# Performance work log

Measured on AMD Instinct MI355X. Metric: run time of the kernel, lower is better.

## Reference

```python
import jax, jax.numpy as jnp
import numpy as np

B, T, C = 256, 512, 128


def setup_inputs() -> dict:
    key = jax.random.key(0)
    k1, k2, k3, k4 = jax.random.split(key, 4)
    emissions = jax.random.normal(k1, (B, T, C), dtype=jnp.float32)
    tags = jax.random.randint(k2, (B, T), 0, C)
    lengths = jax.random.randint(k3, (B,), T // 2, T + 1)
    mask = jnp.arange(T)[None, :] < lengths[:, None]  # [B,T] bool, prefix-true
    transitions = jax.random.uniform(k4, (C, C), minval=-0.1, maxval=0.1, dtype=jnp.float32)
    return {"emissions": emissions, "tags": tags, "mask": mask, "transitions": transitions}


def reference(emissions, tags, mask, transitions):
    # emissions: [B,T,C] float, tags: [B,T] int, mask: [B,T] bool, transitions: [C,C] float
    # ---- log partition (forward algorithm), scan over time ----
    def step(log_alpha, xs):
        emit_t, mask_t = xs  # [B,C], [B]
        # scores[b,i,j] = log_alpha[b,i] + transitions[i,j] + emit_t[b,j]
        scores = log_alpha[:, :, None] + transitions[None, :, :] + emit_t[:, None, :]
        nxt = jax.nn.logsumexp(scores, axis=1)  # [B,C]
        log_alpha = jnp.where(mask_t[:, None], nxt, log_alpha)
        return log_alpha, None

    em_rest = jnp.swapaxes(emissions[:, 1:], 0, 1)  # [T-1,B,C]
    mk_rest = jnp.swapaxes(mask[:, 1:], 0, 1)       # [T-1,B]
    log_alpha, _ = jax.lax.scan(step, emissions[:, 0], (em_rest, mk_rest))
    log_den = jax.nn.logsumexp(log_alpha, axis=1)   # [B]

    # ---- joint log likelihood of gold path ----
    emit_score = jnp.take_along_axis(emissions, tags[..., None], axis=2)[..., 0]  # [B,T]
    maskf = mask.astype(emissions.dtype)
    pair_mask = (mask[:, 1:] & mask[:, :-1]).astype(emissions.dtype)              # [B,T-1]
    trans_score = (transitions[tags[:, :-1], tags[:, 1:]] * pair_mask).sum(axis=1)  # [B]
    log_num = (emit_score * maskf).sum(axis=1) + trans_score

    return jnp.mean(log_den - log_num)
```

## Files before the change

kernel.cpp:

```cpp
#include <hip/hip_runtime.h>

#define BB 256
#define TT 512
#define CC 128
#define G  16
#define NBLK (BB / G)

typedef short short8 __attribute__((ext_vector_type(8)));
typedef float f32x4  __attribute__((ext_vector_type(4)));

__device__ __forceinline__ unsigned f2bf(float v) {
    unsigned u = __float_as_uint(v);
    u += 0x7FFFu + ((u >> 16) & 1u);
    return u >> 16;
}
__device__ __forceinline__ unsigned pack2(float a, float b) {
    return f2bf(a) | (f2bf(b) << 16);
}
__device__ __forceinline__ unsigned umx(unsigned a, unsigned b) { return a > b ? a : b; }

__global__ __launch_bounds__(256, 1)
void crf_forward(const float* __restrict__ em_all,
                 const void* __restrict__ mask,
                 const float* __restrict__ transitions,
                 float* __restrict__ log_den)
{
    const int tid = threadIdx.x;
    const int l = tid & 63, w = tid >> 6;
    const int n = l & 15, g = l >> 4;
    const int bbase = blockIdx.x * G;

    __shared__ __align__(16) unsigned abuf[2][16 * 64];
    __shared__ float finred[4][16];

    auto aidx = [](int nn, int s) -> int {
        return nn * 64 + ((s ^ ((nn & 7) << 4)) >> 1);
    };

    const unsigned char* mb = (const unsigned char*)mask;
    const bool is_u8 = (mb[1] != 0);
    int cnt = 0;
    const int rowbase = (bbase + n) * TT + g * 128;
    if (is_u8) {
        const uint4* mp = (const uint4*)(mb + rowbase);
        #pragma unroll
        for (int k = 0; k < 8; ++k) {
            const uint4 v = mp[k];
            const unsigned s4 = (v.x & 0x01010101u) + (v.y & 0x01010101u)
                              + (v.z & 0x01010101u) + (v.w & 0x01010101u);
            cnt += (int)((s4 * 0x01010101u) >> 24);
        }
    } else {
        const uint4* mp = (const uint4*)((const unsigned*)mask + rowbase);
        #pragma unroll
        for (int k = 0; k < 32; ++k) {
            const uint4 v = mp[k];
            cnt += (v.x ? 1 : 0) + (v.y ? 1 : 0) + (v.z ? 1 : 0) + (v.w ? 1 : 0);
        }
    }
    cnt += __shfl_xor(cnt, 16); cnt += __shfl_xor(cnt, 32);
    const int len_n = cnt;
    int lmx = len_n;
    #pragma unroll
    for (int off = 1; off <= 8; off <<= 1) lmx = max(lmx, __shfl_xor(lmx, off));
    const int len_max = lmx;

    short8 afr[2][4];
    #pragma unroll
    for (int mt = 0; mt < 2; ++mt) {
        #pragma unroll
        for (int kt = 0; kt < 4; ++kt) {
            short8 a;
            #pragma unroll
            for (int e = 0; e < 8; ++e) {
                const int k = 32 * kt + 8 * g + e;
                const int m = 32 * w + 16 * mt + n;
                a[e] = (short)f2bf(__expf(transitions[k * CC + m]));
            }
            afr[mt][kt] = a;
        }
    }

    const float* emb = em_all + (size_t)(bbase + n) * TT * CC;
    const int s0 = 32 * w + 4 * g;
    float av[8]; unsigned pk[4];
    {
        const f32x4 e0 = *(const f32x4*)&emb[s0];
        const f32x4 e1 = *(const f32x4*)&emb[s0 + 16];
        #pragma unroll
        for (int i = 0; i < 4; ++i) { av[i] = __expf(e0[i]); av[4 + i] = __expf(e1[i]); }
        pk[0] = pack2(av[0], av[1]); pk[1] = pack2(av[2], av[3]);
        pk[2] = pack2(av[4], av[5]); pk[3] = pack2(av[6], av[7]);
        *(uint2*)&abuf[0][aidx(n, s0)]      = make_uint2(pk[0], pk[1]);
        *(uint2*)&abuf[0][aidx(n, s0 + 16)] = make_uint2(pk[2], pk[3]);
    }
    f32x4 emc0 = *(const f32x4*)&emb[(size_t)1 * CC + s0];
    f32x4 emc1 = *(const f32x4*)&emb[(size_t)1 * CC + s0 + 16];
    f32x4 emn0 = *(const f32x4*)&emb[(size_t)2 * CC + s0];
    f32x4 emn1 = *(const f32x4*)&emb[(size_t)2 * CC + s0 + 16];
    float logoff = 0.f;

    asm volatile("s_waitcnt lgkmcnt(0)\n\ts_barrier" ::: "memory");

    for (int t = 1; t < len_max; ++t) {
        const int tf = (t + 2 < TT) ? (t + 2) : (TT - 1);
        const f32x4 ef0 = *(const f32x4*)&emb[(size_t)tf * CC + s0];
        const f32x4 ef1 = *(const f32x4*)&emb[(size_t)tf * CC + s0 + 16];

        const unsigned* rbuf = abuf[(t + 1) & 1];
        uint4 rbu[4];
        #pragma unroll
        for (int kt = 0; kt < 4; ++kt)
            rbu[kt] = *(const uint4*)&rbuf[aidx(n, 32 * kt + 8 * g)];

        f32x4 acc0 = {0.f, 0.f, 0.f, 0.f}, acc1 = {0.f, 0.f, 0.f, 0.f};
        #pragma unroll
        for (int kt = 0; kt < 4; ++kt) {
            const short8 bf = __builtin_bit_cast(short8, rbu[kt]);
            acc0 = __builtin_amdgcn_mfma_f32_16x16x32_bf16(afr[0][kt], bf, acc0, 0, 0, 0);
            acc1 = __builtin_amdgcn_mfma_f32_16x16x32_bf16(afr[1][kt], bf, acc1, 0, 0, 0);
        }

        int ex = 0; float scale = 1.0f;
        if ((t & 3) == 0) {
            unsigned mx = 0;
            #pragma unroll
            for (int kt = 0; kt < 4; ++kt) {
                mx = umx(mx, rbu[kt].x & 0xFFFF0000u); mx = umx(mx, rbu[kt].x << 16);
                mx = umx(mx, rbu[kt].y & 0xFFFF0000u); mx = umx(mx, rbu[kt].y << 16);
                mx = umx(mx, rbu[kt].z & 0xFFFF0000u); mx = umx(mx, rbu[kt].z << 16);
                mx = umx(mx, rbu[kt].w & 0xFFFF0000u); mx = umx(mx, rbu[kt].w << 16);
            }
            mx = umx(mx, (unsigned)__shfl_xor((int)mx, 16));
            mx = umx(mx, (unsigned)__shfl_xor((int)mx, 32));
            ex = (int)((mx >> 23) & 255u) - 127;
            scale = __uint_as_float((unsigned)(127 - ex) << 23);
        }

        const bool active = (t < len_n);
        float nv[8];
        #pragma unroll
        for (int i = 0; i < 4; ++i) {
            nv[i]     = acc0[i] * __expf(emc0[i]) * scale;
            nv[4 + i] = acc1[i] * __expf(emc1[i]) * scale;
        }
        if (active) {
            #pragma unroll
            for (int i = 0; i < 8; ++i) av[i] = nv[i];
            pk[0] = pack2(av[0], av[1]); pk[1] = pack2(av[2], av[3]);
            pk[2] = pack2(av[4], av[5]); pk[3] = pack2(av[6], av[7]);
            logoff += (float)ex * 0.69314718f;
        }
        emc0 = emn0; emc1 = emn1; emn0 = ef0; emn1 = ef1;

        unsigned* wbuf = abuf[t & 1];
        *(uint2*)&wbuf[aidx(n, s0)]      = make_uint2(pk[0], pk[1]);
        *(uint2*)&wbuf[aidx(n, s0 + 16)] = make_uint2(pk[2], pk[3]);

        asm volatile("s_waitcnt lgkmcnt(0)\n\ts_barrier" ::: "memory");
    }

    float s = ((av[0] + av[1]) + (av[2] + av[3])) + ((av[4] + av[5]) + (av[6] + av[7]));
    s += __shfl_xor(s, 16); s += __shfl_xor(s, 32);
    if (l < 16) finred[w][l] = s;
    __syncthreads();
    if (w == 0 && l < 16) {
        const float tot = finred[0][l] + finred[1][l] + finred[2][l] + finred[3][l];
        log_den[bbase + l] = logoff + __logf(tot);
    }
}

__device__ __forceinline__ bool mask_at(const void* mask, bool is_u8, int idx) {
    if (is_u8) return ((const unsigned char*)mask)[idx] != 0;
    return ((const int*)mask)[idx] != 0;
}

__global__ __launch_bounds__(256)
void crf_num(const float* __restrict__ em_all,
             const int* __restrict__ tags,
             const void* __restrict__ mask,
             const float* __restrict__ transitions,
             float* __restrict__ log_num)
{
    const int b = blockIdx.x;
    const int j = threadIdx.x;
    const int lane = j & 63;
    const int wid = j >> 6;
    __shared__ float redf[4];

    const unsigned char* mb = (const unsigned char*)mask;
    const bool is_u8 = (mb[1] != 0);

    const float* em = em_all + (size_t)b * TT * CC;
    const int* tg = tags + b * TT;

    float s = 0.f;
    for (int t = j; t < TT; t += 256) {
        if (mask_at(mask, is_u8, b * TT + t)) {
            s += em[t * CC + tg[t]];
            if (t >= 1 && mask_at(mask, is_u8, b * TT + t - 1))
                s += transitions[tg[t - 1] * CC + tg[t]];
        }
    }
    #pragma unroll
    for (int off = 32; off; off >>= 1) s += __shfl_xor(s, off);
    if (lane == 0) redf[wid] = s;
    __syncthreads();
    if (j == 0) log_num[b] = redf[0] + redf[1] + redf[2] + redf[3];
}

__global__ __launch_bounds__(256)
void crf_final(const float* __restrict__ log_den,
               const float* __restrict__ log_num,
               float* __restrict__ out)
{
    const int j = threadIdx.x;
    const int lane = j & 63;
    const int wid = j >> 6;
    __shared__ float redf[4];
    float v = log_den[j] - log_num[j];
    #pragma unroll
    for (int off = 32; off; off >>= 1) v += __shfl_xor(v, off);
    if (lane == 0) redf[wid] = v;
    __syncthreads();
    if (j == 0) out[0] = (redf[0] + redf[1] + redf[2] + redf[3]) * (1.0f / BB);
}

extern "C" void kernel_launch(void* const* d_in, const int* in_sizes, int n_in,
                              void* d_out, int out_size, void* d_ws, size_t ws_size,
                              hipStream_t stream) {
    const float* emissions   = (const float*)d_in[0];
    const int*   tags        = (const int*)d_in[1];
    const void*  mask        = d_in[2];
    const float* transitions = (const float*)d_in[3];
    float* out = (float*)d_out;

    float* log_den = (float*)d_ws;
    float* log_num = log_den + BB;

    crf_forward<<<NBLK, 256, 0, stream>>>(emissions, mask, transitions, log_den);
    crf_num<<<BB, 256, 0, stream>>>(emissions, tags, mask, transitions, log_num);
    crf_final<<<1, 256, 0, stream>>>(log_den, log_num, out);
}
```

Baseline: 257.3 us.

## Pack two sequence groups per block and precompute emission exponentials off critical path

The forward-scan kernel now runs two independent 16-sequence groups per 512-thread block, so there are half as many blocks and two waves share each SIMD. Interleaving those waves is meant to hide MFMA and LDS latency in the serial time loop. The exp of each emission row is now taken when that row is prefetched, not inside the recurrence update. The LDS swizzle pattern also changes. The trade-off is that the block-wide barrier now couples both groups, and the loop runs to the longest length across 32 sequences instead of 16.

```diff
diff --git a/kernel.cpp b/kernel.cpp
--- a/kernel.cpp
+++ b/kernel.cpp
@@ -3,8 +3,8 @@
 #define BB 256
 #define TT 512
 #define CC 128
-#define G  16
-#define NBLK (BB / G)
+#define GPB 2
+#define NBLK (BB / (16 * GPB))
 
 typedef short short8 __attribute__((ext_vector_type(8)));
 typedef float f32x4  __attribute__((ext_vector_type(4)));
@@ -18,8 +18,11 @@
     return f2bf(a) | (f2bf(b) << 16);
 }
 __device__ __forceinline__ unsigned umx(unsigned a, unsigned b) { return a > b ? a : b; }
-
-__global__ __launch_bounds__(256, 1)
+__device__ __forceinline__ f32x4 expv4(f32x4 x) {
+    return f32x4{__expf(x[0]), __expf(x[1]), __expf(x[2]), __expf(x[3])};
+}
+
+__global__ __launch_bounds__(512, 1)
 void crf_forward(const float* __restrict__ em_all,
                  const void* __restrict__ mask,
                  const float* __restrict__ transitions,
@@ -27,14 +30,16 @@
 {
     const int tid = threadIdx.x;
     const int l = tid & 63, w = tid >> 6;
+    const int q = w >> 2, ws = w & 3;
     const int n = l & 15, g = l >> 4;
-    const int bbase = blockIdx.x * G;
-
-    __shared__ __align__(16) unsigned abuf[2][16 * 64];
-    __shared__ float finred[4][16];
+    const int bbase = blockIdx.x * (16 * GPB) + 16 * q;
+
+    __shared__ __align__(16) unsigned abuf[2][GPB][16 * 64];
+    __shared__ float finred[GPB][4][16];
+    __shared__ int lenred[2 * GPB * 4];
 
     auto aidx = [](int nn, int s) -> int {
-        return nn * 64 + ((s ^ ((nn & 7) << 4)) >> 1);
+        return nn * 64 + ((s ^ ((nn & 15) << 3)) >> 1);
     };
 
     const unsigned char* mb = (const unsigned char*)mask;
@@ -63,7 +68,11 @@
     int lmx = len_n;
     #pragma unroll
     for (int off = 1; off <= 8; off <<= 1) lmx = max(lmx, __shfl_xor(lmx, off));
-    const int len_max = lmx;
+    if (l == 0) lenred[w] = lmx;
+    __syncthreads();
+    int len_max = lenred[0];
+    #pragma unroll
+    for (int k = 1; k < 8; ++k) len_max = max(len_max, lenred[k]);
 
     short8 afr[2][4];
     #pragma unroll
@@ -74,7 +83,7 @@
             #pragma unroll
             for (int e = 0; e < 8; ++e) {
                 const int k = 32 * kt + 8 * g + e;
-                const int m = 32 * w + 16 * mt + n;
+                const int m = 32 * ws + 16 * mt + n;
                 a[e] = (short)f2bf(__expf(transitions[k * CC + m]));
             }
             afr[mt][kt] = a;
@@ -82,7 +91,7 @@
     }
 
     const float* emb = em_all + (size_t)(bbase + n) * TT * CC;
-    const int s0 = 32 * w + 4 * g;
+    const int s0 = 32 * ws + 4 * g;
     float av[8]; unsigned pk[4];
     {
         const f32x4 e0 = *(const f32x4*)&emb[s0];
@@ -91,13 +100,13 @@
         for (int i = 0; i < 4; ++i) { av[i] = __expf(e0[i]); av[4 + i] = __expf(e1[i]); }
         pk[0] = pack2(av[0], av[1]); pk[1] = pack2(av[2], av[3]);
         pk[2] = pack2(av[4], av[5]); pk[3] = pack2(av[6], av[7]);
-        *(uint2*)&abuf[0][aidx(n, s0)]      = make_uint2(pk[0], pk[1]);
-        *(uint2*)&abuf[0][aidx(n, s0 + 16)] = make_uint2(pk[2], pk[3]);
-    }
-    f32x4 emc0 = *(const f32x4*)&emb[(size_t)1 * CC + s0];
-    f32x4 emc1 = *(const f32x4*)&emb[(size_t)1 * CC + s0 + 16];
-    f32x4 emn0 = *(const f32x4*)&emb[(size_t)2 * CC + s0];
-    f32x4 emn1 = *(const f32x4*)&emb[(size_t)2 * CC + s0 + 16];
+        *(uint2*)&abuf[0][q][aidx(n, s0)]      = make_uint2(pk[0], pk[1]);
+        *(uint2*)&abuf[0][q][aidx(n, s0 + 16)] = make_uint2(pk[2], pk[3]);
+    }
+    f32x4 emc0 = expv4(*(const f32x4*)&emb[(size_t)1 * CC + s0]);
+    f32x4 emc1 = expv4(*(const f32x4*)&emb[(size_t)1 * CC + s0 + 16]);
+    f32x4 emn0 = expv4(*(const f32x4*)&emb[(size_t)2 * CC + s0]);
+    f32x4 emn1 = expv4(*(const f32x4*)&emb[(size_t)2 * CC + s0 + 16]);
     float logoff = 0.f;
 
     asm volatile("s_waitcnt lgkmcnt(0)\n\ts_barrier" ::: "memory");
@@ -107,7 +116,7 @@
         const f32x4 ef0 = *(const f32x4*)&emb[(size_t)tf * CC + s0];
         const f32x4 ef1 = *(const f32x4*)&emb[(size_t)tf * CC + s0 + 16];
 
-        const unsigned* rbuf = abuf[(t + 1) & 1];
+        const unsigned* rbuf = abuf[(t + 1) & 1][q];
         uint4 rbu[4];
         #pragma unroll
         for (int kt = 0; kt < 4; ++kt)
@@ -141,8 +150,8 @@
         float nv[8];
         #pragma unroll
         for (int i = 0; i < 4; ++i) {
-            nv[i]     = acc0[i] * __expf(emc0[i]) * scale;
-            nv[4 + i] = acc1[i] * __expf(emc1[i]) * scale;
+            nv[i]     = acc0[i] * emc0[i] * scale;
+            nv[4 + i] = acc1[i] * emc1[i] * scale;
         }
         if (active) {
             #pragma unroll
@@ -151,9 +160,9 @@
             pk[2] = pack2(av[4], av[5]); pk[3] = pack2(av[6], av[7]);
             logoff += (float)ex * 0.69314718f;
         }
-        emc0 = emn0; emc1 = emn1; emn0 = ef0; emn1 = ef1;
-
-        unsigned* wbuf = abuf[t & 1];
+        emc0 = emn0; emc1 = emn1; emn0 = expv4(ef0); emn1 = expv4(ef1);
+
+        unsigned* wbuf = abuf[t & 1][q];
         *(uint2*)&wbuf[aidx(n, s0)]      = make_uint2(pk[0], pk[1]);
         *(uint2*)&wbuf[aidx(n, s0 + 16)] = make_uint2(pk[2], pk[3]);
 
@@ -162,10 +171,11 @@
 
     float s = ((av[0] + av[1]) + (av[2] + av[3])) + ((av[4] + av[5]) + (av[6] + av[7]));
     s += __shfl_xor(s, 16); s += __shfl_xor(s, 32);
-    if (l < 16) finred[w][l] = s;
-    __syncthreads();
-    if (w == 0 && l < 16) {
-        const float tot = finred[0][l] + finred[1][l] + finred[2][l] + finred[3][l];
+    if (l < 16) finred[q][ws][l] = s;
+    __syncthreads();
+    if (ws == 0 && l < 16) {
+        const float tot = finred[q][0][l] + finred[q][1][l]
+                        + finred[q][2][l] + finred[q][3][l];
         log_den[bbase + l] = logoff + __logf(tot);
     }
 }
@@ -238,7 +248,7 @@
     float* log_den = (float*)d_ws;
     float* log_num = log_den + BB;
 
-    crf_forward<<<NBLK, 256, 0, stream>>>(emissions, mask, transitions, log_den);
+    crf_forward<<<NBLK, 512, 0, stream>>>(emissions, mask, transitions, log_den);
     crf_num<<<BB, 256, 0, stream>>>(emissions, tags, mask, transitions, log_num);
     crf_final<<<1, 256, 0, stream>>>(log_den, log_num, out);
 }
```

New measurement: 482.0 us. 1.87x slower.

## Process two batch groups per block and precompute exp(emissions) in bf16

Applied to the files above, without the earlier changes.

The forward kernel now handles 32 sequences per block as two interleaved groups, so each timestep issues twice as many independent MFMAs per barrier, and it launches half as many blocks. When the workspace is large enough, a separate pass first writes exp(emissions) as bf16 so the serial scan loop loads half the bytes and skips the per-step exp. Conversions now use the hardware packed bf16 convert, and the masking branches become selects. The cost is an extra full pass over the emissions tensor and fewer blocks on a device with many CUs, which lowers parallelism for what is a latency-bound scan.

```diff
diff --git a/kernel.cpp b/kernel.cpp
--- a/kernel.cpp
+++ b/kernel.cpp
@@ -3,24 +3,71 @@
 #define BB 256
 #define TT 512
 #define CC 128
-#define G  16
-#define NBLK (BB / G)
+#define NBLK (BB / 32)
+#define EEXP_OFF 4096
 
 typedef short short8 __attribute__((ext_vector_type(8)));
 typedef float f32x4  __attribute__((ext_vector_type(4)));
 
-__device__ __forceinline__ unsigned f2bf(float v) {
-    unsigned u = __float_as_uint(v);
-    u += 0x7FFFu + ((u >> 16) & 1u);
-    return u >> 16;
-}
-__device__ __forceinline__ unsigned pack2(float a, float b) {
-    return f2bf(a) | (f2bf(b) << 16);
+__device__ __forceinline__ unsigned cvtpk(float lo, float hi) {
+    unsigned r;
+    asm("v_cvt_pk_bf16_f32 %0, %1, %2" : "=v"(r) : "v"(lo), "v"(hi));
+    return r;
 }
 __device__ __forceinline__ unsigned umx(unsigned a, unsigned b) { return a > b ? a : b; }
-
+__device__ __forceinline__ f32x4 expv4(f32x4 x) {
+    return f32x4{__expf(x[0]), __expf(x[1]), __expf(x[2]), __expf(x[3])};
+}
+__device__ __forceinline__ float bflo(unsigned u) { return __uint_as_float(u << 16); }
+__device__ __forceinline__ float bfhi(unsigned u) { return __uint_as_float(u & 0xFFFF0000u); }
+
+template<bool PRE> struct ERaw { uint2 a, b; };
+template<> struct ERaw<false> { f32x4 a, b; };
+
+template<bool PRE>
+__device__ __forceinline__ ERaw<PRE> eload(const void* base, int idx) {
+    if constexpr (PRE) {
+        const unsigned short* p = (const unsigned short*)base;
+        ERaw<PRE> r;
+        r.a = *(const uint2*)&p[idx];
+        r.b = *(const uint2*)&p[idx + 16];
+        return r;
+    } else {
+        const float* p = (const float*)base;
+        ERaw<PRE> r;
+        r.a = *(const f32x4*)&p[idx];
+        r.b = *(const f32x4*)&p[idx + 16];
+        return r;
+    }
+}
+template<bool PRE>
+__device__ __forceinline__ void econv(const ERaw<PRE>& r, f32x4& e0, f32x4& e1) {
+    if constexpr (PRE) {
+        e0 = f32x4{bflo(r.a.x), bfhi(r.a.x), bflo(r.a.y), bfhi(r.a.y)};
+        e1 = f32x4{bflo(r.b.x), bfhi(r.b.x), bflo(r.b.y), bfhi(r.b.y)};
+    } else {
+        e0 = expv4(r.a);
+        e1 = expv4(r.b);
+    }
+}
+
+__global__ __launch_bounds__(256)
+void crf_expemit(const float* __restrict__ em, unsigned short* __restrict__ ee)
+{
+    const int i = (blockIdx.x * 256 + threadIdx.x) * 8;
+    const f32x4 a = *(const f32x4*)&em[i];
+    const f32x4 b = *(const f32x4*)&em[i + 4];
+    uint4 o;
+    o.x = cvtpk(__expf(a[0]), __expf(a[1]));
+    o.y = cvtpk(__expf(a[2]), __expf(a[3]));
+    o.z = cvtpk(__expf(b[0]), __expf(b[1]));
+    o.w = cvtpk(__expf(b[2]), __expf(b[3]));
+    *(uint4*)&ee[i] = o;
+}
+
+template<bool PRE>
 __global__ __launch_bounds__(256, 1)
-void crf_forward(const float* __restrict__ em_all,
+void crf_forward(const void* __restrict__ em_all,
                  const void* __restrict__ mask,
                  const float* __restrict__ transitions,
                  float* __restrict__ log_den)
@@ -28,42 +75,49 @@
     const int tid = threadIdx.x;
     const int l = tid & 63, w = tid >> 6;
     const int n = l & 15, g = l >> 4;
-    const int bbase = blockIdx.x * G;
-
-    __shared__ __align__(16) unsigned abuf[2][16 * 64];
-    __shared__ float finred[4][16];
+    const int bbase = blockIdx.x * 32;
+
+    __shared__ __align__(16) unsigned abuf[2][2][16 * 64];
+    __shared__ float finred[2][4][16];
+    __shared__ int lenred[4];
 
     auto aidx = [](int nn, int s) -> int {
-        return nn * 64 + ((s ^ ((nn & 7) << 4)) >> 1);
+        return nn * 64 + ((s ^ ((nn & 15) << 3)) >> 1);
     };
 
     const unsigned char* mb = (const unsigned char*)mask;
     const bool is_u8 = (mb[1] != 0);
-    int cnt = 0;
-    const int rowbase = (bbase + n) * TT + g * 128;
-    if (is_u8) {
-        const uint4* mp = (const uint4*)(mb + rowbase);
-        #pragma unroll
-        for (int k = 0; k < 8; ++k) {
-            const uint4 v = mp[k];
-            const unsigned s4 = (v.x & 0x01010101u) + (v.y & 0x01010101u)
-                              + (v.z & 0x01010101u) + (v.w & 0x01010101u);
-            cnt += (int)((s4 * 0x01010101u) >> 24);
-        }
-    } else {
-        const uint4* mp = (const uint4*)((const unsigned*)mask + rowbase);
-        #pragma unroll
-        for (int k = 0; k < 32; ++k) {
-            const uint4 v = mp[k];
-            cnt += (v.x ? 1 : 0) + (v.y ? 1 : 0) + (v.z ? 1 : 0) + (v.w ? 1 : 0);
-        }
-    }
-    cnt += __shfl_xor(cnt, 16); cnt += __shfl_xor(cnt, 32);
-    const int len_n = cnt;
-    int lmx = len_n;
+    int lenA = 0, lenB = 0;
+    #pragma unroll
+    for (int grp = 0; grp < 2; ++grp) {
+        int cnt = 0;
+        const int rowbase = (bbase + 16 * grp + n) * TT + g * 128;
+        if (is_u8) {
+            const uint4* mp = (const uint4*)(mb + rowbase);
+            #pragma unroll
+            for (int k = 0; k < 8; ++k) {
+                const uint4 v = mp[k];
+                const unsigned s4 = (v.x & 0x01010101u) + (v.y & 0x01010101u)
+                                  + (v.z & 0x01010101u) + (v.w & 0x01010101u);
+                cnt += (int)((s4 * 0x01010101u) >> 24);
+            }
+        } else {
+            const uint4* mp = (const uint4*)((const unsigned*)mask + rowbase);
+            #pragma unroll
+            for (int k = 0; k < 32; ++k) {
+                const uint4 v = mp[k];
+                cnt += (v.x ? 1 : 0) + (v.y ? 1 : 0) + (v.z ? 1 : 0) + (v.w ? 1 : 0);
+            }
+        }
+        cnt += __shfl_xor(cnt, 16); cnt += __shfl_xor(cnt, 32);
+        if (grp == 0) lenA = cnt; else lenB = cnt;
+    }
+    int lmx = max(lenA, lenB);
     #pragma unroll
     for (int off = 1; off <= 8; off <<= 1) lmx = max(lmx, __shfl_xor(lmx, off));
-    const int len_max = lmx;
+    if (l == 0) lenred[w] = lmx;
+    __syncthreads();
+    const int len_max = max(max(lenred[0], lenred[1]), max(lenred[2], lenred[3]));
 
     short8 afr[2][4];
     #pragma unroll
@@ -72,101 +126,168 @@
         for (int kt = 0; kt < 4; ++kt) {
             short8 a;
             #pragma unroll
-            for (int e = 0; e < 8; ++e) {
-                const int k = 32 * kt + 8 * g + e;
+            for (int e = 0; e < 4; ++e) {
+                const int k = 32 * kt + 8 * g + 2 * e;
                 const int m = 32 * w + 16 * mt + n;
-                a[e] = (short)f2bf(__expf(transitions[k * CC + m]));
+                const unsigned pk2 = cvtpk(__expf(transitions[k * CC + m]),
+                                           __expf(transitions[(k + 1) * CC + m]));
+                a[2 * e]     = (short)(pk2 & 0xFFFF);
+                a[2 * e + 1] = (short)(pk2 >> 16);
             }
             afr[mt][kt] = a;
         }
     }
 
-    const float* emb = em_all + (size_t)(bbase + n) * TT * CC;
     const int s0 = 32 * w + 4 * g;
-    float av[8]; unsigned pk[4];
+    const size_t strideB = (size_t)TT * CC;
+    const void* embA; const void* embB;
+    if constexpr (PRE) {
+        embA = (const void*)((const unsigned short*)em_all + (size_t)(bbase + n) * strideB);
+        embB = (const void*)((const unsigned short*)em_all + (size_t)(bbase + 16 + n) * strideB);
+    } else {
+        embA = (const void*)((const float*)em_all + (size_t)(bbase + n) * strideB);
+        embB = (const void*)((const float*)em_all + (size_t)(bbase + 16 + n) * strideB);
+    }
+
+    float avA[8], avB[8]; unsigned pkA[4], pkB[4];
     {
-        const f32x4 e0 = *(const f32x4*)&emb[s0];
-        const f32x4 e1 = *(const f32x4*)&emb[s0 + 16];
-        #pragma unroll
-        for (int i = 0; i < 4; ++i) { av[i] = __expf(e0[i]); av[4 + i] = __expf(e1[i]); }
-        pk[0] = pack2(av[0], av[1]); pk[1] = pack2(av[2], av[3]);
-        pk[2] = pack2(av[4], av[5]); pk[3] = pack2(av[6], av[7]);
-        *(uint2*)&abuf[0][aidx(n, s0)]      = make_uint2(pk[0], pk[1]);
-        *(uint2*)&abuf[0][aidx(n, s0 + 16)] = make_uint2(pk[2], pk[3]);
-    }
-    f32x4 emc0 = *(const f32x4*)&emb[(size_t)1 * CC + s0];
-    f32x4 emc1 = *(const f32x4*)&emb[(size_t)1 * CC + s0 + 16];
-    f32x4 emn0 = *(const f32x4*)&emb[(size_t)2 * CC + s0];
-    f32x4 emn1 = *(const f32x4*)&emb[(size_t)2 * CC + s0 + 16];
-    float logoff = 0.f;
-
-    asm volatile("s_waitcnt lgkmcnt(0)\n\ts_barrier" ::: "memory");
+        f32x4 i0, i1;
+        ERaw<PRE> r0 = eload<PRE>(embA, 0 * CC + s0);
+        econv<PRE>(r0, i0, i1);
+        if constexpr (!PRE) {  }
+        #pragma unroll
+        for (int i = 0; i < 4; ++i) { avA[i] = i0[i]; avA[4 + i] = i1[i]; }
+        r0 = eload<PRE>(embB, 0 * CC + s0);
+        econv<PRE>(r0, i0, i1);
+        #pragma unroll
+        for (int i = 0; i < 4; ++i) { avB[i] = i0[i]; avB[4 + i] = i1[i]; }
+    }
+    pkA[0] = cvtpk(avA[0], avA[1]); pkA[1] = cvtpk(avA[2], avA[3]);
+    pkA[2] = cvtpk(avA[4], avA[5]); pkA[3] = cvtpk(avA[6], avA[7]);
+    pkB[0] = cvtpk(avB[0], avB[1]); pkB[1] = cvtpk(avB[2], avB[3]);
+    pkB[2] = cvtpk(avB[4], avB[5]); pkB[3] = cvtpk(avB[6], avB[7]);
+    *(uint2*)&abuf[0][0][aidx(n, s0)]      = make_uint2(pkA[0], pkA[1]);
+    *(uint2*)&abuf[0][0][aidx(n, s0 + 16)] = make_uint2(pkA[2], pkA[3]);
+    *(uint2*)&abuf[0][1][aidx(n, s0)]      = make_uint2(pkB[0], pkB[1]);
+    *(uint2*)&abuf[0][1][aidx(n, s0 + 16)] = make_uint2(pkB[2], pkB[3]);
+
+    f32x4 ecA0, ecA1, ecB0, ecB1;
+    {
+        ERaw<PRE> r1 = eload<PRE>(embA, 1 * CC + s0);
+        econv<PRE>(r1, ecA0, ecA1);
+        r1 = eload<PRE>(embB, 1 * CC + s0);
+        econv<PRE>(r1, ecB0, ecB1);
+    }
+    ERaw<PRE> rawA = eload<PRE>(embA, ((2 < TT) ? 2 : TT - 1) * CC + s0);
+    ERaw<PRE> rawB = eload<PRE>(embB, ((2 < TT) ? 2 : TT - 1) * CC + s0);
+    float logoffA = 0.f, logoffB = 0.f;
+
+    __syncthreads();
 
     for (int t = 1; t < len_max; ++t) {
         const int tf = (t + 2 < TT) ? (t + 2) : (TT - 1);
-        const f32x4 ef0 = *(const f32x4*)&emb[(size_t)tf * CC + s0];
-        const f32x4 ef1 = *(const f32x4*)&emb[(size_t)tf * CC + s0 + 16];
-
-        const unsigned* rbuf = abuf[(t + 1) & 1];
-        uint4 rbu[4];
-        #pragma unroll
-        for (int kt = 0; kt < 4; ++kt)
-            rbu[kt] = *(const uint4*)&rbuf[aidx(n, 32 * kt + 8 * g)];
-
-        f32x4 acc0 = {0.f, 0.f, 0.f, 0.f}, acc1 = {0.f, 0.f, 0.f, 0.f};
+        const ERaw<PRE> ldA = eload<PRE>(embA, tf * CC + s0);
+        const ERaw<PRE> ldB = eload<PRE>(embB, tf * CC + s0);
+
+        const unsigned* rbA = abuf[(t + 1) & 1][0];
+        const unsigned* rbB = abuf[(t + 1) & 1][1];
+        uint4 rA[4], rB[4];
+        #pragma unroll
+        for (int kt = 0; kt < 4; ++kt) rA[kt] = *(const uint4*)&rbA[aidx(n, 32 * kt + 8 * g)];
+        #pragma unroll
+        for (int kt = 0; kt < 4; ++kt) rB[kt] = *(const uint4*)&rbB[aidx(n, 32 * kt + 8 * g)];
+
+        f32x4 aA0 = {0,0,0,0}, aA1 = {0,0,0,0}, aB0 = {0,0,0,0}, aB1 = {0,0,0,0};
         #pragma unroll
         for (int kt = 0; kt < 4; ++kt) {
-            const short8 bf = __builtin_bit_cast(short8, rbu[kt]);
-            acc0 = __builtin_amdgcn_mfma_f32_16x16x32_bf16(afr[0][kt], bf, acc0, 0, 0, 0);
-            acc1 = __builtin_amdgcn_mfma_f32_16x16x32_bf16(afr[1][kt], bf, acc1, 0, 0, 0);
-        }
-
-        int ex = 0; float scale = 1.0f;
+            const short8 bfA = __builtin_bit_cast(short8, rA[kt]);
+            const short8 bfB = __builtin_bit_cast(short8, rB[kt]);
+            aA0 = __builtin_amdgcn_mfma_f32_16x16x32_bf16(afr[0][kt], bfA, aA0, 0, 0, 0);
+            aA1 = __builtin_amdgcn_mfma_f32_16x16x32_bf16(afr[1][kt], bfA, aA1, 0, 0, 0);
+            aB0 = __builtin_amdgcn_mfma_f32_16x16x32_bf16(afr[0][kt], bfB, aB0, 0, 0, 0);
+            aB1 = __builtin_amdgcn_mfma_f32_16x16x32_bf16(afr[1][kt], bfB, aB1, 0, 0, 0);
+        }
+
+        float scA = 1.0f, scB = 1.0f, exfA = 0.f, exfB = 0.f;
         if ((t & 3) == 0) {
-            unsigned mx = 0;
+            unsigned mxA = 0, mxB = 0;
             #pragma unroll
             for (int kt = 0; kt < 4; ++kt) {
-                mx = umx(mx, rbu[kt].x & 0xFFFF0000u); mx = umx(mx, rbu[kt].x << 16);
-                mx = umx(mx, rbu[kt].y & 0xFFFF0000u); mx = umx(mx, rbu[kt].y << 16);
-                mx = umx(mx, rbu[kt].z & 0xFFFF0000u); mx = umx(mx, rbu[kt].z << 16);
-                mx = umx(mx, rbu[kt].w & 0xFFFF0000u); mx = umx(mx, rbu[kt].w << 16);
+                mxA = umx(mxA, umx(umx(rA[kt].x & 0xFFFF0000u, rA[kt].x << 16),
+                                   umx(rA[kt].y & 0xFFFF0000u, rA[kt].y << 16)));
+                mxA = umx(mxA, umx(umx(rA[kt].z & 0xFFFF0000u, rA[kt].z << 16),
+                                   umx(rA[kt].w & 0xFFFF0000u, rA[kt].w << 16)));
+                mxB = umx(mxB, umx(umx(rB[kt].x & 0xFFFF0000u, rB[kt].x << 16),
+                                   umx(rB[kt].y & 0xFFFF0000u, rB[kt].y << 16)));
+                mxB = umx(mxB, umx(umx(rB[kt].z & 0xFFFF0000u, rB[kt].z << 16),
+                                   umx(rB[kt].w & 0xFFFF0000u, rB[kt].w << 16)));
             }
-            mx = umx(mx, (unsigned)__shfl_xor((int)mx, 16));
-            mx = umx(mx, (unsigned)__shfl_xor((int)mx, 32));
-            ex = (int)((mx >> 23) & 255u) - 127;
-            scale = __uint_as_float((unsigned)(127 - ex) << 23);
-        }
-
-        const bool active = (t < len_n);
-        float nv[8];
+            mxA = umx(mxA, (unsigned)__shfl_xor((int)mxA, 16));
+            mxA = umx(mxA, (unsigned)__shfl_xor((int)mxA, 32));
+            mxB = umx(mxB, (unsigned)__shfl_xor((int)mxB, 16));
+            mxB = umx(mxB, (unsigned)__shfl_xor((int)mxB, 32));
+            const int exA = (int)((mxA >> 23) & 255u) - 127;
+            const int exB = (int)((mxB >> 23) & 255u) - 127;
+            scA = __uint_as_float((unsigned)(127 - exA) << 23);
+            scB = __uint_as_float((unsigned)(127 - exB) << 23);
+            exfA = (float)exA; exfB = (float)exB;
+        }
+
+        const bool actA = (t < lenA), actB = (t < lenB);
+        float nvA[8], nvB[8];
         #pragma unroll
         for (int i = 0; i < 4; ++i) {
-            nv[i]     = acc0[i] * __expf(emc0[i]) * scale;
-            nv[4 + i] = acc1[i] * __expf(emc1[i]) * scale;
-        }
-        if (active) {
-            #pragma unroll
-            for (int i = 0; i < 8; ++i) av[i] = nv[i];
-            pk[0] = pack2(av[0], av[1]); pk[1] = pack2(av[2], av[3]);
-            pk[2] = pack2(av[4], av[5]); pk[3] = pack2(av[6], av[7]);
-            logoff += (float)ex * 0.69314718f;
-        }
-        emc0 = emn0; emc1 = emn1; emn0 = ef0; emn1 = ef1;
-
-        unsigned* wbuf = abuf[t & 1];
-        *(uint2*)&wbuf[aidx(n, s0)]      = make_uint2(pk[0], pk[1]);
-        *(uint2*)&wbuf[aidx(n, s0 + 16)] = make_uint2(pk[2], pk[3]);
+            nvA[i]     = aA0[i] * ecA0[i] * scA;
+            nvA[4 + i] = aA1[i] * ecA1[i] * scA;
+            nvB[i]     = aB0[i] * ecB0[i] * scB;
+            nvB[4 + i] = aB1[i] * ecB1[i] * scB;
+        }
+        #pragma unroll
+        for (int i = 0; i < 8; ++i) {
+            avA[i] = actA ? nvA[i] : avA[i];
+            avB[i] = actB ? nvB[i] : avB[i];
+        }
+        unsigned npA[4], npB[4];
+        npA[0] = cvtpk(nvA[0], nvA[1]); npA[1] = cvtpk(nvA[2], nvA[3]);
+        npA[2] = cvtpk(nvA[4], nvA[5]); npA[3] = cvtpk(nvA[6], nvA[7]);
+        npB[0] = cvtpk(nvB[0], nvB[1]); npB[1] = cvtpk(nvB[2], nvB[3]);
+        npB[2] = cvtpk(nvB[4], nvB[5]); npB[3] = cvtpk(nvB[6], nvB[7]);
+        #pragma unroll
+        for (int i = 0; i < 4; ++i) {
+            pkA[i] = actA ? npA[i] : pkA[i];
+            pkB[i] = actB ? npB[i] : pkB[i];
+        }
+        logoffA += actA ? exfA * 0.6931471805599453f : 0.f;
+        logoffB += actB ? exfB * 0.6931471805599453f : 0.f;
+
+        econv<PRE>(rawA, ecA0, ecA1);
+        econv<PRE>(rawB, ecB0, ecB1);
+        rawA = ldA; rawB = ldB;
+
+        unsigned* wbA = abuf[t & 1][0];
+        unsigned* wbB = abuf[t & 1][1];
+        *(uint2*)&wbA[aidx(n, s0)]      = make_uint2(pkA[0], pkA[1]);
+        *(uint2*)&wbA[aidx(n, s0 + 16)] = make_uint2(pkA[2], pkA[3]);
+        *(uint2*)&wbB[aidx(n, s0)]      = make_uint2(pkB[0], pkB[1]);
+        *(uint2*)&wbB[aidx(n, s0 + 16)] = make_uint2(pkB[2], pkB[3]);
 
         asm volatile("s_waitcnt lgkmcnt(0)\n\ts_barrier" ::: "memory");
     }
 
-    float s = ((av[0] + av[1]) + (av[2] + av[3])) + ((av[4] + av[5]) + (av[6] + av[7]));
-    s += __shfl_xor(s, 16); s += __shfl_xor(s, 32);
-    if (l < 16) finred[w][l] = s;
+    float sA = ((avA[0] + avA[1]) + (avA[2] + avA[3])) + ((avA[4] + avA[5]) + (avA[6] + avA[7]));
+    float sB = ((avB[0] + avB[1]) + (avB[2] + avB[3])) + ((avB[4] + avB[5]) + (avB[6] + avB[7]));
+    sA += __shfl_xor(sA, 16); sA += __shfl_xor(sA, 32);
+    sB += __shfl_xor(sB, 16); sB += __shfl_xor(sB, 32);
+    __syncthreads();
+    if (l < 16) { finred[0][w][l] = sA; finred[1][w][l] = sB; }
     __syncthreads();
     if (w == 0 && l < 16) {
-        const float tot = finred[0][l] + finred[1][l] + finred[2][l] + finred[3][l];
-        log_den[bbase + l] = logoff + __logf(tot);
+        const float tot = finred[0][0][l] + finred[0][1][l] + finred[0][2][l] + finred[0][3][l];
+        log_den[bbase + l] = logoffA + __logf(tot);
+    }
+    if (w == 1 && l < 16) {
+        const float tot = finred[1][0][l] + finred[1][1][l] + finred[1][2][l] + finred[1][3][l];
+        log_den[bbase + 16 + l] = logoffB + __logf(tot);
     }
 }
 
@@ -238,7 +359,16 @@
     float* log_den = (float*)d_ws;
     float* log_num = log_den + BB;
 
-    crf_forward<<<NBLK, 256, 0, stream>>>(emissions, mask, transitions, log_den);
+    const size_t eexp_bytes = (size_t)BB * TT * CC * 2;
+    const bool pre = ws_size >= (size_t)EEXP_OFF + eexp_bytes;
+
+    if (pre) {
+        unsigned short* eexp = (unsigned short*)((char*)d_ws + EEXP_OFF);
+        crf_expemit<<<(BB * TT * CC) / 2048, 256, 0, stream>>>(emissions, eexp);
+        crf_forward<true><<<NBLK, 256, 0, stream>>>(eexp, mask, transitions, log_den);
+    } else {
+        crf_forward<false><<<NBLK, 256, 0, stream>>>(emissions, mask, transitions, log_den);
+    }
     crf_num<<<BB, 256, 0, stream>>>(emissions, tags, mask, transitions, log_num);
     crf_final<<<1, 256, 0, stream>>>(log_den, log_num, out);
 }
```

Measured after the change: 376.0 us. 1.46x slower.
